# Optimization experiments

Measured on AMD Instinct MI355X. Metric: run time of the kernel, lower is better.

## Reference

```python
import jax, jax.numpy as jnp
import numpy as np

MARGIN = 0.5
EPS = 1e-8  # torch CosineSimilarity eps


def setup_inputs() -> dict:
    key = jax.random.key(0)
    k1, k2 = jax.random.split(key)
    line_end_embeddings = jax.random.normal(k1, (4096, 32, 256), dtype=jnp.float32)
    rhyme_scheme = jax.random.randint(k2, (4096, 32), 0, 4, dtype=jnp.int32)
    return {"line_end_embeddings": line_end_embeddings, "rhyme_scheme": rhyme_scheme}


def reference(line_end_embeddings, rhyme_scheme):
    b, n, d = line_end_embeddings.shape
    # cosine similarity with torch-style eps clamping on norms
    norms = jnp.maximum(jnp.linalg.norm(line_end_embeddings, axis=-1, keepdims=True), EPS)
    unit = line_end_embeddings / norms                       # [b, n, d]
    sims = jnp.einsum("bid,bjd->bij", unit, unit)            # [b, n, n]
    same = rhyme_scheme[:, :, None] == rhyme_scheme[:, None, :]  # [b, n, n]
    per_pair = jnp.where(same, 1.0 - sims, jax.nn.relu(sims - MARGIN))
    # only pairs i < j (strict upper triangle)
    upper = jnp.triu(jnp.ones((n, n), dtype=bool), k=1)
    total = jnp.sum(per_pair * upper[None, :, :])
    count = b * (n * (n - 1) // 2)
    return total / max(count, 1)
```

## Files before the change

### kernel.cpp

```cpp
#include <hip/hip_runtime.h>
#include <hip/hip_bf16.h>
#include <stdint.h>


typedef short bf16x8 __attribute__((ext_vector_type(8)));
typedef float f32x4  __attribute__((ext_vector_type(4)));

#define MARGIN 0.5f
#define EPS_NORM 1e-8f
#define NPAIR_INV (1.0f / 2031616.0f)

static __device__ __forceinline__ short f2bf(float f) {
    unsigned u = __float_as_uint(f);
    u += 0x7fffu + ((u >> 16) & 1u);
    return (short)(u >> 16);
}

__global__ __launch_bounds__(256, 8) void rhyme_loss_kernel(
    const float* __restrict__ emb,
    const int*   __restrict__ sch,
    float*       __restrict__ part)
{
    __shared__ f32x4 s_acc[3][3][64];
    __shared__ float s_diag[32];
    __shared__ float s_inv[32];
    __shared__ int   s_sch[32];

    const int t    = threadIdx.x;
    const int wv   = t >> 6;
    const int lane = t & 63;
    const int b    = blockIdx.x;

    const int q = lane >> 4;
    const int c = lane & 15;

    if (t < 32)
        s_sch[t] = sch[(size_t)b * 32 + t];

    const float* base0 = emb + (size_t)b * 8192 + (size_t)c * 256 + wv * 64 + q * 8;
    const float* base1 = base0 + 16 * 256;

    f32x4 acc00 = {0.f, 0.f, 0.f, 0.f};
    f32x4 acc01 = {0.f, 0.f, 0.f, 0.f};
    f32x4 acc11 = {0.f, 0.f, 0.f, 0.f};

    #pragma unroll
    for (int kc = 0; kc < 64; kc += 32) {
        float4 a0 = *(const float4*)(base0 + kc);
        float4 a1 = *(const float4*)(base0 + kc + 4);
        float4 b0 = *(const float4*)(base1 + kc);
        float4 b1 = *(const float4*)(base1 + kc + 4);

        bf16x8 f0, f1;
        f0[0] = f2bf(a0.x); f0[1] = f2bf(a0.y); f0[2] = f2bf(a0.z); f0[3] = f2bf(a0.w);
        f0[4] = f2bf(a1.x); f0[5] = f2bf(a1.y); f0[6] = f2bf(a1.z); f0[7] = f2bf(a1.w);
        f1[0] = f2bf(b0.x); f1[1] = f2bf(b0.y); f1[2] = f2bf(b0.z); f1[3] = f2bf(b0.w);
        f1[4] = f2bf(b1.x); f1[5] = f2bf(b1.y); f1[6] = f2bf(b1.z); f1[7] = f2bf(b1.w);

        acc00 = __builtin_amdgcn_mfma_f32_16x16x32_bf16(f0, f0, acc00, 0, 0, 0);
        acc01 = __builtin_amdgcn_mfma_f32_16x16x32_bf16(f0, f1, acc01, 0, 0, 0);
        acc11 = __builtin_amdgcn_mfma_f32_16x16x32_bf16(f1, f1, acc11, 0, 0, 0);
    }

    if (wv != 0) {
        s_acc[wv - 1][0][lane] = acc00;
        s_acc[wv - 1][1][lane] = acc01;
        s_acc[wv - 1][2][lane] = acc11;
    }
    __syncthreads();

    if (wv == 0) {
        #pragma unroll
        for (int p = 0; p < 3; ++p) {
            acc00 += s_acc[p][0][lane];
            acc01 += s_acc[p][1][lane];
            acc11 += s_acc[p][2][lane];
        }

        const int dreg = c - 4 * q;
        if (dreg >= 0 && dreg < 4) {
            s_diag[c]      = acc00[dreg];
            s_diag[16 + c] = acc11[dreg];
        }
        __builtin_amdgcn_wave_barrier();
        if (lane < 32)
            s_inv[lane] = 1.0f / fmaxf(sqrtf(s_diag[lane]), EPS_NORM);
        __builtin_amdgcn_wave_barrier();

        const float invj0 = s_inv[c];
        const float invj1 = s_inv[16 + c];
        const int   sj0   = s_sch[c];
        const int   sj1   = s_sch[16 + c];

        float sum = 0.0f;
        #pragma unroll
        for (int r = 0; r < 4; ++r) {
            const int   i0    = q * 4 + r;
            const float inv_i = s_inv[i0];
            const int   si    = s_sch[i0];

            {
                float sim = acc01[r] * inv_i * invj1;
                sum += (si == sj1) ? (1.0f - sim) : fmaxf(sim - MARGIN, 0.0f);
            }
            if (i0 < c) {
                float sim = acc00[r] * inv_i * invj0;
                sum += (si == sj0) ? (1.0f - sim) : fmaxf(sim - MARGIN, 0.0f);
                float sim2 = acc11[r] * s_inv[16 + i0] * invj1;
                sum += (s_sch[16 + i0] == sj1) ? (1.0f - sim2)
                                               : fmaxf(sim2 - MARGIN, 0.0f);
            }
        }

        #pragma unroll
        for (int off = 32; off > 0; off >>= 1)
            sum += __shfl_down(sum, off, 64);

        if (lane == 0)
            part[b] = sum;
    }
}

__global__ __launch_bounds__(256) void reduce_kernel(
    const float* __restrict__ part,
    float*       __restrict__ out)
{
    __shared__ float s[4];
    const int t = threadIdx.x;
    float sum = 0.0f;
    const float4* p4 = (const float4*)part;
    #pragma unroll
    for (int i = 0; i < 4; ++i) {
        float4 v = p4[t + 256 * i];
        sum += (v.x + v.y) + (v.z + v.w);
    }
    #pragma unroll
    for (int off = 32; off > 0; off >>= 1)
        sum += __shfl_down(sum, off, 64);
    if ((t & 63) == 0) s[t >> 6] = sum;
    __syncthreads();
    if (t == 0)
        out[0] = ((s[0] + s[1]) + (s[2] + s[3])) * NPAIR_INV;
}

extern "C" void kernel_launch(void* const* d_in, const int* in_sizes, int n_in,
                              void* d_out, int out_size, void* d_ws, size_t ws_size,
                              hipStream_t stream) {
    const float* emb  = (const float*)d_in[0];
    const int*   sch  = (const int*)d_in[1];
    float*       out  = (float*)d_out;
    float*       part = (float*)d_ws;

    rhyme_loss_kernel<<<dim3(4096), dim3(256), 0, stream>>>(emb, sch, part);
    reduce_kernel<<<dim3(1), dim3(256), 0, stream>>>(part, out);
}
```

Measured before the change: 190.2 us.

## Assign one batch per wave instead of splitting K across four waves

Each wave now handles one whole batch element and loops over the full 256-wide feature dimension. Previously four waves each took a quarter of K for the same batch, and partial accumulators were combined through shared memory. This removes the cross-wave LDS reduction and the block-wide __syncthreads, and lets all waves do the epilogue instead of only wave 0. In exchange each wave issues more loads serially, so less memory-level parallelism per batch, and the grid shrinks to 1024 blocks.

```diff
diff --git a/kernel.cpp b/kernel.cpp
--- a/kernel.cpp
+++ b/kernel.cpp
@@ -1,5 +1,4 @@
 #include <hip/hip_runtime.h>
-#include <hip/hip_bf16.h>
 #include <stdint.h>
 
 
@@ -21,23 +20,23 @@
     const int*   __restrict__ sch,
     float*       __restrict__ part)
 {
-    __shared__ f32x4 s_acc[3][3][64];
-    __shared__ float s_diag[32];
-    __shared__ float s_inv[32];
-    __shared__ int   s_sch[32];
+    __shared__ float s_diag[4][32];
+    __shared__ float s_inv[4][32];
+    __shared__ int   s_sch[4][32];
 
     const int t    = threadIdx.x;
     const int wv   = t >> 6;
     const int lane = t & 63;
-    const int b    = blockIdx.x;
+    const int b    = (blockIdx.x << 2) | wv;
 
     const int q = lane >> 4;
     const int c = lane & 15;
 
-    if (t < 32)
-        s_sch[t] = sch[(size_t)b * 32 + t];
+    if (lane < 32)
+        s_sch[wv][lane] = sch[(size_t)b * 32 + lane];
+    __builtin_amdgcn_wave_barrier();
 
-    const float* base0 = emb + (size_t)b * 8192 + (size_t)c * 256 + wv * 64 + q * 8;
+    const float* base0 = emb + (size_t)b * 8192 + (size_t)c * 256 + q * 8;
     const float* base1 = base0 + 16 * 256;
 
     f32x4 acc00 = {0.f, 0.f, 0.f, 0.f};
@@ -45,7 +44,7 @@
     f32x4 acc11 = {0.f, 0.f, 0.f, 0.f};
 
     #pragma unroll
-    for (int kc = 0; kc < 64; kc += 32) {
+    for (int kc = 0; kc < 256; kc += 32) {
         float4 a0 = *(const float4*)(base0 + kc);
         float4 a1 = *(const float4*)(base0 + kc + 4);
         float4 b0 = *(const float4*)(base1 + kc);
@@ -62,63 +61,47 @@
         acc11 = __builtin_amdgcn_mfma_f32_16x16x32_bf16(f1, f1, acc11, 0, 0, 0);
     }
 
-    if (wv != 0) {
-        s_acc[wv - 1][0][lane] = acc00;
-        s_acc[wv - 1][1][lane] = acc01;
-        s_acc[wv - 1][2][lane] = acc11;
+    const int dreg = c - 4 * q;
+    if (dreg >= 0 && dreg < 4) {
+        s_diag[wv][c]      = acc00[dreg];
+        s_diag[wv][16 + c] = acc11[dreg];
     }
-    __syncthreads();
+    __builtin_amdgcn_wave_barrier();
+    if (lane < 32)
+        s_inv[wv][lane] = 1.0f / fmaxf(sqrtf(s_diag[wv][lane]), EPS_NORM);
+    __builtin_amdgcn_wave_barrier();
 
-    if (wv == 0) {
-        #pragma unroll
-        for (int p = 0; p < 3; ++p) {
-            acc00 += s_acc[p][0][lane];
-            acc01 += s_acc[p][1][lane];
-            acc11 += s_acc[p][2][lane];
+    const float invj0 = s_inv[wv][c];
+    const float invj1 = s_inv[wv][16 + c];
+    const int   sj0   = s_sch[wv][c];
+    const int   sj1   = s_sch[wv][16 + c];
+
+    float sum = 0.0f;
+    #pragma unroll
+    for (int r = 0; r < 4; ++r) {
+        const int   i0    = q * 4 + r;
+        const float inv_i = s_inv[wv][i0];
+        const int   si    = s_sch[wv][i0];
+
+        {
+            float sim = acc01[r] * inv_i * invj1;
+            sum += (si == sj1) ? (1.0f - sim) : fmaxf(sim - MARGIN, 0.0f);
         }
+        if (i0 < c) {
+            float sim = acc00[r] * inv_i * invj0;
+            sum += (si == sj0) ? (1.0f - sim) : fmaxf(sim - MARGIN, 0.0f);
+            float sim2 = acc11[r] * s_inv[wv][16 + i0] * invj1;
+            sum += (s_sch[wv][16 + i0] == sj1) ? (1.0f - sim2)
+                                               : fmaxf(sim2 - MARGIN, 0.0f);
+        }
+    }
 
-        const int dreg = c - 4 * q;
-        if (dreg >= 0 && dreg < 4) {
-            s_diag[c]      = acc00[dreg];
-            s_diag[16 + c] = acc11[dreg];
-        }
-        __builtin_amdgcn_wave_barrier();
-        if (lane < 32)
-            s_inv[lane] = 1.0f / fmaxf(sqrtf(s_diag[lane]), EPS_NORM);
-        __builtin_amdgcn_wave_barrier();
+    #pragma unroll
+    for (int off = 32; off > 0; off >>= 1)
+        sum += __shfl_down(sum, off, 64);
 
-        const float invj0 = s_inv[c];
-        const float invj1 = s_inv[16 + c];
-        const int   sj0   = s_sch[c];
-        const int   sj1   = s_sch[16 + c];
-
-        float sum = 0.0f;
-        #pragma unroll
-        for (int r = 0; r < 4; ++r) {
-            const int   i0    = q * 4 + r;
-            const float inv_i = s_inv[i0];
-            const int   si    = s_sch[i0];
-
-            {
-                float sim = acc01[r] * inv_i * invj1;
-                sum += (si == sj1) ? (1.0f - sim) : fmaxf(sim - MARGIN, 0.0f);
-            }
-            if (i0 < c) {
-                float sim = acc00[r] * inv_i * invj0;
-                sum += (si == sj0) ? (1.0f - sim) : fmaxf(sim - MARGIN, 0.0f);
-                float sim2 = acc11[r] * s_inv[16 + i0] * invj1;
-                sum += (s_sch[16 + i0] == sj1) ? (1.0f - sim2)
-                                               : fmaxf(sim2 - MARGIN, 0.0f);
-            }
-        }
-
-        #pragma unroll
-        for (int off = 32; off > 0; off >>= 1)
-            sum += __shfl_down(sum, off, 64);
-
-        if (lane == 0)
-            part[b] = sum;
-    }
+    if (lane == 0)
+        part[b] = sum;
 }
 
 __global__ __launch_bounds__(256) void reduce_kernel(
@@ -151,6 +134,6 @@
     float*       out  = (float*)d_out;
     float*       part = (float*)d_ws;
 
-    rhyme_loss_kernel<<<dim3(4096), dim3(256), 0, stream>>>(emb, sch, part);
+    rhyme_loss_kernel<<<dim3(1024), dim3(256), 0, stream>>>(emb, sch, part);
     reduce_kernel<<<dim3(1), dim3(256), 0, stream>>>(part, out);
 }
```

Measured after the change: 196.8 us. +3.5%, slower.
